# Performance work log

Measured on AMD Instinct MI355X. Metric: run time of the kernel, lower is better.

Reference implementation:

```python
import jax, jax.numpy as jnp
import numpy as np

K = 20          # n_neighbors
EPS = 1e-5      # batchnorm eps
SLOPE = 0.2     # leaky relu slope (DGCNN default)


def _bn_lrelu(x, axes):
    # batch-norm (per-batch stats, gamma=1, beta=0) + LeakyReLU(0.2)
    m = jnp.mean(x, axis=axes, keepdims=True)
    v = jnp.var(x, axis=axes, keepdims=True)
    return jax.nn.leaky_relu((x - m) * jax.lax.rsqrt(v + EPS), SLOPE)


def _knn(x_cf, k):
    # x_cf: (B, C, N) -> idx (B, N, k) of k nearest neighbors (incl. self)
    inner = jnp.einsum('bcn,bcm->bnm', x_cf, x_cf)
    sq = jnp.sum(x_cf * x_cf, axis=1)                  # (B, N)
    neg_d = 2.0 * inner - sq[:, :, None] - sq[:, None, :]
    return jax.lax.top_k(neg_d, k)[1]


def _gather(x_nl, idx):
    # x_nl: (B, N, C), idx: (B, N, k) -> (B, N, k, C) neighbor features
    return jnp.take_along_axis(x_nl[:, :, None, :], idx[..., None], axis=1)


def setup_inputs() -> dict:
    key = jax.random.key(0)
    ks = jax.random.split(key, 11)
    B, N, C = 16, 2048, 3
    dims = [64, 64, 128, 256]
    feat_dim = 1024

    def w(k, o, i):
        return jax.random.normal(k, (o, i), jnp.float32) / np.sqrt(i)

    return {
        'x': jax.random.normal(ks[0], (B, N, C), jnp.float32),
        'w_edge': w(ks[1], dims[0], 2 * C),
        'b_edge': jnp.zeros((dims[0],), jnp.float32),
        'w1': w(ks[2], dims[1], dims[0]),
        'b1': jnp.zeros((dims[1],), jnp.float32),
        'w2': w(ks[3], dims[2], dims[1]),
        'b2': jnp.zeros((dims[2],), jnp.float32),
        'w3': w(ks[4], dims[3], dims[2]),
        'b3': jnp.zeros((dims[3],), jnp.float32),
        'w_final': w(ks[5], feat_dim, sum(dims)),
        'b_final': jnp.zeros((feat_dim,), jnp.float32),
    }


def reference(x, w_edge, b_edge, w1, b1, w2, b2, w3, b3, w_final, b_final):
    # x: (B, N, 3) point cloud
    x_cf = jnp.transpose(x, (0, 2, 1))                 # (B, 3, N)
    idx = _knn(x_cf, K)                                # (B, N, k) -- graph built once

    # get_graph_features: edge feature = concat(neighbor - center, center)
    nb = _gather(x, idx)                               # (B, N, k, 3)
    ctr = jnp.broadcast_to(x[:, :, None, :], nb.shape)
    feat = jnp.concatenate([nb - ctr, ctr], axis=-1)   # (B, N, k, 6)

    # EdgeConvLayer: 1x1 conv2d + BN + LeakyReLU, then max over neighbors
    h = jnp.einsum('oc,bnkc->bonk', w_edge, feat) + b_edge[None, :, None, None]
    h = _bn_lrelu(h, (0, 2, 3))
    h = jnp.max(h, axis=3)                             # (B, 64, N)

    xs = [h]
    for w, b in ((w1, b1), (w2, b2), (w3, b3)):
        # graph_max_pooling with reused kNN indices
        g = jnp.max(_gather(jnp.transpose(h, (0, 2, 1)), idx), axis=2)  # (B, N, C)
        h = jnp.einsum('oc,bnc->bon', w, g) + b[None, :, None]          # 1x1 conv1d
        h = _bn_lrelu(h, (0, 2))
        xs.append(h)

    h_cat = jnp.concatenate(xs, axis=1)                # (B, 512, N)
    out = jnp.einsum('oc,bcn->bon', w_final, h_cat) + b_final[None, :, None]
    return jnp.max(out, axis=2)                        # (B, 1024)
```

## Files before the change

### kernel.cpp

```cpp
#include <hip/hip_runtime.h>
#include <hip/hip_bf16.h>
#include <math.h>

#define B_ 16
#define N_ 2048
#define KNN 20
#define SLOPE 0.2f
#define EPS_ 1e-5f

#define SEG 8
#define SEGLEN (N_ / SEG)
#define QPB 64
#define CAP 64

typedef __attribute__((ext_vector_type(8))) short short8;
typedef __attribute__((ext_vector_type(4))) float float4v;

__global__ __launch_bounds__(256, 2) void knn_kernel(const float* __restrict__ x,
                                                     int* __restrict__ idx,
                                                     const float* __restrict__ w_edge,
                                                     const float* __restrict__ b_edge,
                                                     float* __restrict__ cat,
                                                     double* __restrict__ stats) {
    __shared__ float4 pts4[N_];
    __shared__ union {
        float thr[QPB * 24];
        int sidx[QPB * KNN];
    } u2;
    __shared__ float tq[QPB];
    __shared__ int cnt[QPB];
    __shared__ float lv[QPB * CAP];
    __shared__ int   li[QPB * CAP];
    __shared__ float ws[64 * 6];
    __shared__ float bs[64];
    __shared__ float s_sum[64], s_sq[64];

    const int b = blockIdx.x >> 5;
    const int qb = blockIdx.x & 31;
    const float* xb = x + (size_t)b * N_ * 3;
    for (int i = threadIdx.x; i < N_; i += 256) {
        float xv = xb[i * 3], yv = xb[i * 3 + 1], zv = xb[i * 3 + 2];
        pts4[i] = make_float4(xv, yv, zv, xv * xv + yv * yv + zv * zv);
    }
    for (int i = threadIdx.x; i < 64 * 6; i += 256) ws[i] = w_edge[i];
    if (threadIdx.x < QPB) {
        cnt[threadIdx.x] = 0;
        bs[threadIdx.x] = b_edge[threadIdx.x];
        s_sum[threadIdx.x] = 0.f; s_sq[threadIdx.x] = 0.f;
    }
    __syncthreads();

    const int s = threadIdx.x >> 5;
    const int qs = threadIdx.x & 31;
    const int q0 = qs * 2, q1 = q0 + 1;
    const int n0 = qb * QPB + q0;
    const float4 pa = pts4[n0];
    const float4 pb = pts4[n0 + 1];
    const int m0 = s * SEGLEN;

    float ca[8], cb[8];
#pragma unroll
    for (int c = 0; c < 8; ++c) {
        float va0 = -INFINITY, va1 = -INFINITY;
        float vb0 = -INFINITY, vb1 = -INFINITY;
        for (int g = 0; g < 4; ++g) {
            float4 r[8];
#pragma unroll
            for (int j = 0; j < 8; ++j) r[j] = pts4[m0 + c * 32 + g * 8 + j];
#pragma unroll
            for (int j = 0; j < 8; ++j) {
                const float da = 2.f * (pa.x * r[j].x + pa.y * r[j].y + pa.z * r[j].z)
                                 - pa.w - r[j].w;
                const float db = 2.f * (pb.x * r[j].x + pb.y * r[j].y + pb.z * r[j].z)
                                 - pb.w - r[j].w;
                if (j & 1) { va1 = fmaxf(va1, da); vb1 = fmaxf(vb1, db); }
                else       { va0 = fmaxf(va0, da); vb0 = fmaxf(vb0, db); }
            }
        }
        ca[c] = fmaxf(va0, va1); cb[c] = fmaxf(vb0, vb1);
    }
    {
        float t0 = -INFINITY, t1 = -INFINITY, t2 = -INFINITY;
        float u0 = -INFINITY, u1 = -INFINITY, u2v = -INFINITY;
#pragma unroll
        for (int c = 0; c < 8; ++c) {
            float v = ca[c];
            float r0 = fminf(t0, v); t0 = fmaxf(t0, v);
            float r1 = fminf(t1, r0); t1 = fmaxf(t1, r0);
            t2 = fmaxf(t2, r1);
            float w = cb[c];
            float s0 = fminf(u0, w); u0 = fmaxf(u0, w);
            float s1 = fminf(u1, s0); u1 = fmaxf(u1, s0);
            u2v = fmaxf(u2v, s1);
        }
        u2.thr[q0 * 24 + s * 3 + 0] = t0;
        u2.thr[q0 * 24 + s * 3 + 1] = t1;
        u2.thr[q0 * 24 + s * 3 + 2] = t2;
        u2.thr[q1 * 24 + s * 3 + 0] = u0;
        u2.thr[q1 * 24 + s * 3 + 1] = u1;
        u2.thr[q1 * 24 + s * 3 + 2] = u2v;
    }
    __syncthreads();

    if (threadIdx.x < QPB) {
        const int qq = threadIdx.x;
        float s0 = INFINITY, s1 = INFINITY, s2 = INFINITY, s3 = INFINITY, s4 = INFINITY;
#pragma unroll
        for (int j = 0; j < 24; ++j) {
            float c = u2.thr[qq * 24 + j];
            float u;
            u = fminf(s0, c); c = fmaxf(s0, c); s0 = u;
            u = fminf(s1, c); c = fmaxf(s1, c); s1 = u;
            u = fminf(s2, c); c = fmaxf(s2, c); s2 = u;
            u = fminf(s3, c); c = fmaxf(s3, c); s3 = u;
            s4 = fminf(s4, c);
        }
        tq[qq] = s4 - (fabsf(s4) * 1e-6f + 1e-6f);
    }
    __syncthreads();

    const float ta = tq[q0];
    const float tb = tq[q1];
    for (int g = 0; g < 32; ++g) {
        float4 r[8];
#pragma unroll
        for (int j = 0; j < 8; ++j) r[j] = pts4[m0 + g * 8 + j];
#pragma unroll
        for (int j = 0; j < 8; ++j) {
            const int m = m0 + g * 8 + j;
            const float da = 2.f * (pa.x * r[j].x + pa.y * r[j].y + pa.z * r[j].z)
                             - pa.w - r[j].w;
            const float db = 2.f * (pb.x * r[j].x + pb.y * r[j].y + pb.z * r[j].z)
                             - pb.w - r[j].w;
            if (da >= ta) {
                int pos = atomicAdd(&cnt[q0], 1);
                if (pos < CAP) { lv[q0 * CAP + pos] = da; li[q0 * CAP + pos] = m; }
            }
            if (db >= tb) {
                int pos = atomicAdd(&cnt[q1], 1);
                if (pos < CAP) { lv[q1 * CAP + pos] = db; li[q1 * CAP + pos] = m; }
            }
        }
    }
    __syncthreads();

    if (threadIdx.x < QPB) {
        const int qq = threadIdx.x;
        const int nn = qb * QPB + qq;
        int* op = idx + (size_t)(b * N_ + nn) * KNN;
        float vals[KNN]; int inds[KNN];
#pragma unroll
        for (int j = 0; j < KNN; ++j) { vals[j] = -INFINITY; inds[j] = 0; }
        const int c = cnt[qq];
        if (c <= CAP) {
            for (int j = 0; j < c; ++j) {
                const float v = lv[qq * CAP + j];
                if (v > vals[KNN - 1]) {
                    float cv = v; int ci = li[qq * CAP + j];
#pragma unroll
                    for (int k = 0; k < KNN; ++k) {
                        const bool sw = cv > vals[k];
                        const float tv = vals[k]; const int ti = inds[k];
                        vals[k] = sw ? cv : tv;  inds[k] = sw ? ci : ti;
                        cv      = sw ? tv : cv;  ci      = sw ? ti : ci;
                    }
                }
            }
        } else {
            const float4 pq2 = pts4[nn];
            for (int m = 0; m < N_; ++m) {
                const float4 p = pts4[m];
                const float d = 2.f * (pq2.x * p.x + pq2.y * p.y + pq2.z * p.z)
                                - pq2.w - p.w;
                if (d > vals[KNN - 1]) {
                    float cv = d; int ci = m;
#pragma unroll
                    for (int k = 0; k < KNN; ++k) {
                        const bool sw = cv > vals[k];
                        const float tv = vals[k]; const int ti = inds[k];
                        vals[k] = sw ? cv : tv;  inds[k] = sw ? ci : ti;
                        cv      = sw ? tv : cv;  ci      = sw ? ti : ci;
                    }
                }
            }
        }
#pragma unroll
        for (int j = 0; j < KNN; ++j) {
            op[j] = inds[j];
            u2.sidx[qq * KNN + j] = inds[j];
        }
    }
    __syncthreads();

    {
        const int p = threadIdx.x >> 2;
        const int cg = threadIdx.x & 3;
        const int n = qb * QPB + p;
        const float4 ctr = pts4[n];
        const float cx = ctr.x, cy = ctr.y, cz = ctr.z;

        float maxv[16], sum[16], sq[16];
#pragma unroll
        for (int i = 0; i < 16; ++i) { maxv[i] = -INFINITY; sum[i] = 0.f; sq[i] = 0.f; }

        for (int k = 0; k < KNN; ++k) {
            const int j = u2.sidx[p * KNN + k];
            const float4 nb = pts4[j];
            const float dx = nb.x - cx, dy = nb.y - cy, dz = nb.z - cz;
#pragma unroll
            for (int i = 0; i < 16; ++i) {
                const int o = cg * 16 + i;
                const float* wr = &ws[o * 6];
                float h = bs[o] + wr[0] * dx + wr[1] * dy + wr[2] * dz
                                + wr[3] * cx + wr[4] * cy + wr[5] * cz;
                sum[i] += h; sq[i] += h * h;
                maxv[i] = fmaxf(maxv[i], h);
            }
        }

        float* cp = cat + (size_t)(b * N_ + n) * 512 + cg * 16;
#pragma unroll
        for (int i4 = 0; i4 < 4; ++i4)
            *(float4*)&cp[i4 * 4] = make_float4(maxv[i4 * 4], maxv[i4 * 4 + 1],
                                                maxv[i4 * 4 + 2], maxv[i4 * 4 + 3]);
#pragma unroll
        for (int i = 0; i < 16; ++i) {
            atomicAdd(&s_sum[cg * 16 + i], sum[i]);
            atomicAdd(&s_sq[cg * 16 + i], sq[i]);
        }
    }
    __syncthreads();
    if (threadIdx.x < 64) {
        atomicAdd(&stats[threadIdx.x], (double)s_sum[threadIdx.x]);
        atomicAdd(&stats[64 + threadIdx.x], (double)s_sq[threadIdx.x]);
    }
}

__global__ __launch_bounds__(256) void wconv_kernel(const float* __restrict__ w,
                                                    __hip_bfloat16* __restrict__ wb) {
    int t = blockIdx.x * 256 + threadIdx.x;
    wb[t] = __float2bfloat16(w[t]);
}

template <int CIN, int COUT, int PT>
__global__ __launch_bounds__(256) void layer_kernel(float* __restrict__ cat,
                                                    const int* __restrict__ idx,
                                                    const float* __restrict__ w,
                                                    const float* __restrict__ bias,
                                                    const double* __restrict__ stats_in,
                                                    double invcnt_in,
                                                    double* __restrict__ stats_out,
                                                    int off_in, int off_out) {
    constexpr int P = 64;
    constexpr int LDC = CIN + 4;
    constexpr int WS = COUT + 4;
    constexpr int NCG = CIN / 4;
    constexpr int PPAR = 256 / NCG;
    constexpr int NOG = COUT / 4;
    static_assert(NOG * (P / PT) == 256, "thread mapping");

    __shared__ float g[P * LDC];
    __shared__ float wt[16 * WS];
    __shared__ float s_sum[COUT], s_sq[COUT];

    const int b = blockIdx.x & 15;
    const int pb = blockIdx.x >> 4;
    const int pt0 = b * N_ + pb * P;

    {
        const int cg = threadIdx.x % NCG;
        const int pp = threadIdx.x / NCG;
        float mean[4], inv[4];
#pragma unroll
        for (int j = 0; j < 4; ++j) {
            const double mu = stats_in[cg * 4 + j] * invcnt_in;
            const double e2 = stats_in[CIN + cg * 4 + j] * invcnt_in;
            const float var = (float)(e2 - mu * mu);
            mean[j] = (float)mu;
            inv[j] = rsqrtf(var + EPS_);
        }
        for (int p = pp; p < P; p += PPAR) {
            const int* ip = idx + (size_t)(pt0 + p) * KNN;
            float4 m = make_float4(-INFINITY, -INFINITY, -INFINITY, -INFINITY);
#pragma unroll
            for (int k = 0; k < KNN; ++k) {
                const int j = ip[k];
                const float4 v = *(const float4*)&cat[(size_t)(b * N_ + j) * 512 + off_in + cg * 4];
                m.x = fmaxf(m.x, v.x); m.y = fmaxf(m.y, v.y);
                m.z = fmaxf(m.z, v.z); m.w = fmaxf(m.w, v.w);
            }
            float4 r;
            r.x = (m.x - mean[0]) * inv[0]; r.x = r.x >= 0.f ? r.x : SLOPE * r.x;
            r.y = (m.y - mean[1]) * inv[1]; r.y = r.y >= 0.f ? r.y : SLOPE * r.y;
            r.z = (m.z - mean[2]) * inv[2]; r.z = r.z >= 0.f ? r.z : SLOPE * r.z;
            r.w = (m.w - mean[3]) * inv[3]; r.w = r.w >= 0.f ? r.w : SLOPE * r.w;
            *(float4*)&g[p * LDC + cg * 4] = r;
        }
    }
    if (threadIdx.x < COUT) { s_sum[threadIdx.x] = 0.f; s_sq[threadIdx.x] = 0.f; }

    const int og = threadIdx.x % NOG;
    const int pg = threadIdx.x / NOG;
    const int o0 = og * 4, p0 = pg * PT;

    float acc[4][PT];
#pragma unroll
    for (int i = 0; i < 4; ++i)
#pragma unroll
        for (int j = 0; j < PT; ++j) acc[i][j] = 0.f;

    for (int c0 = 0; c0 < CIN; c0 += 16) {
        __syncthreads();
        for (int i = threadIdx.x; i < COUT * 16; i += 256) {
            int o = i >> 4, cc = i & 15;
            wt[cc * WS + o] = w[(size_t)o * CIN + c0 + cc];
        }
        __syncthreads();
#pragma unroll
        for (int ccq = 0; ccq < 4; ++ccq) {
            const float4 w0 = *(const float4*)&wt[(ccq * 4 + 0) * WS + o0];
            const float4 w1 = *(const float4*)&wt[(ccq * 4 + 1) * WS + o0];
            const float4 w2 = *(const float4*)&wt[(ccq * 4 + 2) * WS + o0];
            const float4 w3 = *(const float4*)&wt[(ccq * 4 + 3) * WS + o0];
#pragma unroll
            for (int p = 0; p < PT; ++p) {
                const float4 gv = *(const float4*)&g[(p0 + p) * LDC + c0 + ccq * 4];
                acc[0][p] += w0.x * gv.x; acc[0][p] += w1.x * gv.y;
                acc[0][p] += w2.x * gv.z; acc[0][p] += w3.x * gv.w;
                acc[1][p] += w0.y * gv.x; acc[1][p] += w1.y * gv.y;
                acc[1][p] += w2.y * gv.z; acc[1][p] += w3.y * gv.w;
                acc[2][p] += w0.z * gv.x; acc[2][p] += w1.z * gv.y;
                acc[2][p] += w2.z * gv.z; acc[2][p] += w3.z * gv.w;
                acc[3][p] += w0.w * gv.x; acc[3][p] += w1.w * gv.y;
                acc[3][p] += w2.w * gv.z; acc[3][p] += w3.w * gv.w;
            }
        }
    }

    const float4 bv = *(const float4*)&bias[o0];
    float lsum[4] = {0.f, 0.f, 0.f, 0.f}, lsq[4] = {0.f, 0.f, 0.f, 0.f};
#pragma unroll
    for (int p = 0; p < PT; ++p) {
        float4 hv;
        hv.x = acc[0][p] + bv.x; hv.y = acc[1][p] + bv.y;
        hv.z = acc[2][p] + bv.z; hv.w = acc[3][p] + bv.w;
        lsum[0] += hv.x; lsq[0] += hv.x * hv.x;
        lsum[1] += hv.y; lsq[1] += hv.y * hv.y;
        lsum[2] += hv.z; lsq[2] += hv.z * hv.z;
        lsum[3] += hv.w; lsq[3] += hv.w * hv.w;
        *(float4*)&cat[(size_t)(pt0 + p0 + p) * 512 + off_out + o0] = hv;
    }
#pragma unroll
    for (int i = 0; i < 4; ++i) {
        atomicAdd(&s_sum[o0 + i], lsum[i]);
        atomicAdd(&s_sq[o0 + i], lsq[i]);
    }
    __syncthreads();
    if (threadIdx.x < COUT) {
        atomicAdd(&stats_out[threadIdx.x], (double)s_sum[threadIdx.x]);
        atomicAdd(&stats_out[COUT + threadIdx.x], (double)s_sq[threadIdx.x]);
    }
}

__global__ __launch_bounds__(256) void bnconv_kernel(const float* __restrict__ cat,
                                                     const double* __restrict__ stats,
                                                     unsigned short* __restrict__ catb,
                                                     double ik, double in_) {
    const int t = blockIdx.x * 256 + threadIdx.x;
    const int pn = t >> 7;
    const int c = (t & 127) * 4;

    const double* sp; const double* qp; double icnt;
    if (c < 64)       { sp = stats + c;             qp = stats + 64 + c;        icnt = ik; }
    else if (c < 128) { sp = stats + 128 + (c - 64);  qp = stats + 192 + (c - 64);  icnt = in_; }
    else if (c < 256) { sp = stats + 256 + (c - 128); qp = stats + 384 + (c - 128); icnt = in_; }
    else              { sp = stats + 512 + (c - 256); qp = stats + 768 + (c - 256); icnt = in_; }

    const float4 v = *(const float4*)&cat[(size_t)pn * 512 + c];
    float r[4]; const float vv[4] = {v.x, v.y, v.z, v.w};
#pragma unroll
    for (int j = 0; j < 4; ++j) {
        const double mu = sp[j] * icnt;
        const double e2 = qp[j] * icnt;
        const float var = (float)(e2 - mu * mu);
        const float inv = rsqrtf(var + EPS_);
        float x = (vv[j] - (float)mu) * inv;
        r[j] = x >= 0.f ? x : SLOPE * x;
    }
    ushort4 o;
    __hip_bfloat16 h0 = __float2bfloat16(r[0]); o.x = *(unsigned short*)&h0;
    __hip_bfloat16 h1 = __float2bfloat16(r[1]); o.y = *(unsigned short*)&h1;
    __hip_bfloat16 h2 = __float2bfloat16(r[2]); o.z = *(unsigned short*)&h2;
    __hip_bfloat16 h3 = __float2bfloat16(r[3]); o.w = *(unsigned short*)&h3;
    *(ushort4*)&catb[(size_t)pn * 512 + c] = o;
}

__global__ __launch_bounds__(256) void final_mfma_kernel(const short* __restrict__ catb,
                                                         const short* __restrict__ wb,
                                                         const float* __restrict__ bias,
                                                         float* __restrict__ partial) {
    constexpr int LDK = 72;
    __shared__ short As[128 * LDK];
    __shared__ short Bs[128 * LDK];
    __shared__ float red[256];

    const int ob = blockIdx.x;
    const int pblk = blockIdx.y;
    const int pt0 = pblk * 128;

    const int wid = threadIdx.x >> 6;
    const int lane = threadIdx.x & 63;
    const int wm = wid >> 1, wn = wid & 1;
    const int lm = lane & 15, g = lane >> 4;

    const int srow = threadIdx.x >> 1;
    const int scg = (threadIdx.x & 1) * 32;
    const short* ga = catb + (size_t)(pt0 + srow) * 512 + scg;
    const short* gb = wb + (size_t)(ob * 128 + srow) * 512 + scg;
    short* la = As + srow * LDK + scg;
    short* lb = Bs + srow * LDK + scg;

    float4v acc[4][4];
#pragma unroll
    for (int i = 0; i < 4; ++i)
#pragma unroll
        for (int j = 0; j < 4; ++j) acc[i][j] = {0.f, 0.f, 0.f, 0.f};

    short8 ra[4], rb[4];
#pragma unroll
    for (int j = 0; j < 4; ++j) {
        ra[j] = *(const short8*)(ga + j * 8);
        rb[j] = *(const short8*)(gb + j * 8);
    }

    for (int step = 0; step < 8; ++step) {
        __syncthreads();
#pragma unroll
        for (int j = 0; j < 4; ++j) {
            *(short8*)(la + j * 8) = ra[j];
            *(short8*)(lb + j * 8) = rb[j];
        }
        __syncthreads();
        if (step < 7) {
            const int c1 = (step + 1) * 64;
#pragma unroll
            for (int j = 0; j < 4; ++j) {
                ra[j] = *(const short8*)(ga + c1 + j * 8);
                rb[j] = *(const short8*)(gb + c1 + j * 8);
            }
        }
#pragma unroll
        for (int kk = 0; kk < 2; ++kk) {
            short8 a[4], b[4];
#pragma unroll
            for (int t = 0; t < 4; ++t) {
                a[t] = *(const short8*)&As[(wm * 64 + t * 16 + lm) * LDK + kk * 32 + g * 8];
                b[t] = *(const short8*)&Bs[(wn * 64 + t * 16 + lm) * LDK + kk * 32 + g * 8];
            }
#pragma unroll
            for (int mt = 0; mt < 4; ++mt)
#pragma unroll
                for (int nt = 0; nt < 4; ++nt)
                    acc[mt][nt] = __builtin_amdgcn_mfma_f32_16x16x32_bf16(
                        a[mt], b[nt], acc[mt][nt], 0, 0, 0);
        }
    }

    float cm[4];
#pragma unroll
    for (int nt = 0; nt < 4; ++nt) {
        float m = -INFINITY;
#pragma unroll
        for (int mt = 0; mt < 4; ++mt)
#pragma unroll
            for (int r = 0; r < 4; ++r) m = fmaxf(m, acc[mt][nt][r]);
        m = fmaxf(m, __shfl_xor(m, 16, 64));
        m = fmaxf(m, __shfl_xor(m, 32, 64));
        cm[nt] = m;
    }
    __syncthreads();
    if (lane < 16) {
#pragma unroll
        for (int nt = 0; nt < 4; ++nt)
            red[wm * 128 + wn * 64 + nt * 16 + lane] = cm[nt];
    }
    __syncthreads();
    if (threadIdx.x < 128) {
        const int o = threadIdx.x;
        float v = fmaxf(red[o], red[128 + o]) + bias[ob * 128 + o];
        partial[(size_t)pblk * 1024 + ob * 128 + o] = v;
    }
}

__global__ __launch_bounds__(256) void reduce_kernel(const float* __restrict__ partial,
                                                     float* __restrict__ out) {
    int t = blockIdx.x * 256 + threadIdx.x;
    int b = t >> 10, o = t & 1023;
    float m = -INFINITY;
#pragma unroll 4
    for (int i = 0; i < 16; ++i)
        m = fmaxf(m, partial[(size_t)((b * 16 + i) * 1024) + o]);
    out[t] = m;
}

extern "C" void kernel_launch(void* const* d_in, const int* in_sizes, int n_in,
                              void* d_out, int out_size, void* d_ws, size_t ws_size,
                              hipStream_t stream) {
    const float* x = (const float*)d_in[0];
    const float* w_edge = (const float*)d_in[1];
    const float* b_edge = (const float*)d_in[2];
    const float* w1 = (const float*)d_in[3];
    const float* b1 = (const float*)d_in[4];
    const float* w2 = (const float*)d_in[5];
    const float* b2 = (const float*)d_in[6];
    const float* w3 = (const float*)d_in[7];
    const float* b3 = (const float*)d_in[8];
    const float* w_final = (const float*)d_in[9];
    const float* b_final = (const float*)d_in[10];
    float* out = (float*)d_out;

    char* ws = (char*)d_ws;
    int* idx = (int*)ws;
    float* cat = (float*)(ws + 2621440);
    float* partial = (float*)(ws + 69730304);
    double* stats = (double*)(ws + 70778880);
    __hip_bfloat16* catb = (__hip_bfloat16*)(ws + 70787072);
    __hip_bfloat16* wb = (__hip_bfloat16*)(ws + 104341504);

    double* st_e = stats;
    double* st_1 = stats + 128;
    double* st_2 = stats + 256;
    double* st_3 = stats + 512;
    const double ik = 1.0 / ((double)B_ * N_ * KNN);
    const double in_ = 1.0 / ((double)B_ * N_);

    hipMemsetAsync(stats, 0, 1024 * sizeof(double), stream);
    wconv_kernel<<<2048, 256, 0, stream>>>(w_final, wb);

    knn_kernel<<<B_ * 32, 256, 0, stream>>>(x, idx, w_edge, b_edge, cat, st_e);
    layer_kernel<64, 64, 4><<<(B_ * N_) / 64, 256, 0, stream>>>(
        cat, idx, w1, b1, st_e, ik, st_1, 0, 64);
    layer_kernel<64, 128, 8><<<(B_ * N_) / 64, 256, 0, stream>>>(
        cat, idx, w2, b2, st_1, in_, st_2, 64, 128);
    layer_kernel<128, 256, 16><<<(B_ * N_) / 64, 256, 0, stream>>>(
        cat, idx, w3, b3, st_2, in_, st_3, 128, 256);
    bnconv_kernel<<<(B_ * N_ * 128) / 256, 256, 0, stream>>>(
        cat, stats, (unsigned short*)catb, ik, in_);
    final_mfma_kernel<<<dim3(8, 256), 256, 0, stream>>>((const short*)catb, (const short*)wb,
                                                        b_final, partial);
    reduce_kernel<<<64, 256, 0, stream>>>(partial, out);
}
```

Baseline: 357.5 us.

## Shrink kNN candidate LDS, hoist center term, retile final GEMM grid

The kNN candidate buffer now keeps only 16-bit indices and recomputes distances during selection. This cuts LDS use so launch bounds can raise occupancy to 3 blocks per CU. The edge-conv loop hoists the bias and center-weight terms out of the neighbor loop. The final GEMM uses a 1D grid with a swizzled block mapping so blocks sharing a point tile run together, aiming at better cache reuse. In exchange the candidate pass does extra LDS reads and arithmetic, and the tighter register limit risks spills.

```diff
diff --git a/kernel.cpp b/kernel.cpp
--- a/kernel.cpp
+++ b/kernel.cpp
@@ -16,7 +16,7 @@
 typedef __attribute__((ext_vector_type(8))) short short8;
 typedef __attribute__((ext_vector_type(4))) float float4v;
 
-__global__ __launch_bounds__(256, 2) void knn_kernel(const float* __restrict__ x,
+__global__ __launch_bounds__(256, 3) void knn_kernel(const float* __restrict__ x,
                                                      int* __restrict__ idx,
                                                      const float* __restrict__ w_edge,
                                                      const float* __restrict__ b_edge,
@@ -29,8 +29,7 @@
     } u2;
     __shared__ float tq[QPB];
     __shared__ int cnt[QPB];
-    __shared__ float lv[QPB * CAP];
-    __shared__ int   li[QPB * CAP];
+    __shared__ unsigned short li[QPB * CAP];
     __shared__ float ws[64 * 6];
     __shared__ float bs[64];
     __shared__ float s_sum[64], s_sq[64];
@@ -134,11 +133,11 @@
                              - pb.w - r[j].w;
             if (da >= ta) {
                 int pos = atomicAdd(&cnt[q0], 1);
-                if (pos < CAP) { lv[q0 * CAP + pos] = da; li[q0 * CAP + pos] = m; }
+                if (pos < CAP) li[q0 * CAP + pos] = (unsigned short)m;
             }
             if (db >= tb) {
                 int pos = atomicAdd(&cnt[q1], 1);
-                if (pos < CAP) { lv[q1 * CAP + pos] = db; li[q1 * CAP + pos] = m; }
+                if (pos < CAP) li[q1 * CAP + pos] = (unsigned short)m;
             }
         }
     }
@@ -148,15 +147,19 @@
         const int qq = threadIdx.x;
         const int nn = qb * QPB + qq;
         int* op = idx + (size_t)(b * N_ + nn) * KNN;
+        const float4 pq2 = pts4[nn];
         float vals[KNN]; int inds[KNN];
 #pragma unroll
         for (int j = 0; j < KNN; ++j) { vals[j] = -INFINITY; inds[j] = 0; }
         const int c = cnt[qq];
         if (c <= CAP) {
             for (int j = 0; j < c; ++j) {
-                const float v = lv[qq * CAP + j];
+                const int m = li[qq * CAP + j];
+                const float4 p = pts4[m];
+                const float v = 2.f * (pq2.x * p.x + pq2.y * p.y + pq2.z * p.z)
+                                - pq2.w - p.w;
                 if (v > vals[KNN - 1]) {
-                    float cv = v; int ci = li[qq * CAP + j];
+                    float cv = v; int ci = m;
 #pragma unroll
                     for (int k = 0; k < KNN; ++k) {
                         const bool sw = cv > vals[k];
@@ -167,7 +170,6 @@
                 }
             }
         } else {
-            const float4 pq2 = pts4[nn];
             for (int m = 0; m < N_; ++m) {
                 const float4 p = pts4[m];
                 const float d = 2.f * (pq2.x * p.x + pq2.y * p.y + pq2.z * p.z)
@@ -199,9 +201,14 @@
         const float4 ctr = pts4[n];
         const float cx = ctr.x, cy = ctr.y, cz = ctr.z;
 
-        float maxv[16], sum[16], sq[16];
-#pragma unroll
-        for (int i = 0; i < 16; ++i) { maxv[i] = -INFINITY; sum[i] = 0.f; sq[i] = 0.f; }
+        float co[16], maxv[16], sum[16], sq[16];
+#pragma unroll
+        for (int i = 0; i < 16; ++i) {
+            const int o = cg * 16 + i;
+            const float* wr = &ws[o * 6];
+            co[i] = bs[o] + wr[3] * cx + wr[4] * cy + wr[5] * cz;
+            maxv[i] = -INFINITY; sum[i] = 0.f; sq[i] = 0.f;
+        }
 
         for (int k = 0; k < KNN; ++k) {
             const int j = u2.sidx[p * KNN + k];
@@ -209,10 +216,8 @@
             const float dx = nb.x - cx, dy = nb.y - cy, dz = nb.z - cz;
 #pragma unroll
             for (int i = 0; i < 16; ++i) {
-                const int o = cg * 16 + i;
-                const float* wr = &ws[o * 6];
-                float h = bs[o] + wr[0] * dx + wr[1] * dy + wr[2] * dz
-                                + wr[3] * cx + wr[4] * cy + wr[5] * cz;
+                const float* wr = &ws[(cg * 16 + i) * 6];
+                float h = co[i] + wr[0] * dx + wr[1] * dy + wr[2] * dz;
                 sum[i] += h; sq[i] += h * h;
                 maxv[i] = fmaxf(maxv[i], h);
             }
@@ -404,8 +409,10 @@
     __shared__ short Bs[128 * LDK];
     __shared__ float red[256];
 
-    const int ob = blockIdx.x;
-    const int pblk = blockIdx.y;
+    const int bid = blockIdx.x;
+    const int plo = bid & 7;
+    const int ob = (bid >> 3) & 7;
+    const int pblk = ((bid >> 6) << 3) | plo;
     const int pt0 = pblk * 128;
 
     const int wid = threadIdx.x >> 6;
@@ -546,7 +553,7 @@
         cat, idx, w3, b3, st_2, in_, st_3, 128, 256);
     bnconv_kernel<<<(B_ * N_ * 128) / 256, 256, 0, stream>>>(
         cat, stats, (unsigned short*)catb, ik, in_);
-    final_mfma_kernel<<<dim3(8, 256), 256, 0, stream>>>((const short*)catb, (const short*)wb,
-                                                        b_final, partial);
+    final_mfma_kernel<<<2048, 256, 0, stream>>>((const short*)catb, (const short*)wb,
+                                                b_final, partial);
     reduce_kernel<<<64, 256, 0, stream>>>(partial, out);
 }
```

After: 351.8 us. About the same (-1.6%).
